# Kernel optimization log

Hardware: AMD Instinct MI355X
Metric: run time of the kernel (lower is better)

Reference implementation:

```python
import jax, jax.numpy as jnp
import numpy as np

TOP_K = 8


def setup_inputs() -> dict:
    key = jax.random.key(0)
    ks = jax.random.split(key, 8)
    B, S, H, BD, N, VBD = 4, 2048, 2048, 256, 256, 256
    return {
        "hidden_states": jax.random.normal(ks[0], (B, S, H), jnp.float32),
        "primary_attention_output": jax.random.normal(ks[1], (B, S, H), jnp.float32),
        "q_proj_w": jax.random.normal(ks[2], (BD, H), jnp.float32) / np.sqrt(H),
        "slot_keys": jax.random.normal(ks[3], (N, BD), jnp.float32),
        "slot_values": jax.random.normal(ks[4], (N, H), jnp.float32),
        "reliability": jax.random.uniform(ks[5], (N,), jnp.float32, 1e-3, 1.0),
        "value_down_w": jax.random.normal(ks[6], (VBD, H), jnp.float32) * 0.1 / np.sqrt(H),
        "value_up_w": jax.random.normal(ks[7], (H, VBD), jnp.float32) * 0.1 / np.sqrt(VBD),
    }


def reference(hidden_states, primary_attention_output, q_proj_w, slot_keys,
              slot_values, reliability, value_down_w, value_up_w):
    B, S, H = hidden_states.shape
    BD = q_proj_w.shape[0]
    # query = q_proj(hidden_states): [B,S,BD]
    query = jnp.einsum("bsh,dh->bsd", hidden_states, q_proj_w)
    # gate-chain scoring: query . slot_keys scaled, plus log-reliability mask
    rel_mask = jnp.log(jnp.clip(reliability, 1e-10))            # [N]
    scores = jnp.einsum("bsd,nd->bsn", query, slot_keys) / jnp.sqrt(
        jnp.asarray(BD, query.dtype)) + rel_mask                # [B,S,N]
    top_scores, top_idx = jax.lax.top_k(scores, TOP_K)          # [B,S,K]
    attn = jax.nn.softmax(top_scores, axis=-1)                  # [B,S,K]
    final_gate = jax.nn.sigmoid(top_scores[..., 0])             # [B,S]
    # slot-pool gather + weighted sum of values (irregular access)
    vals = slot_values[top_idx]                                 # [B,S,K,H]
    aux = jnp.einsum("bsk,bskh->bsh", attn, vals)               # [B,S,H]
    # low-rank value projection with GELU
    aux = jnp.einsum("bsh,vh->bsv", aux, value_down_w)
    aux = jax.nn.gelu(aux)
    aux = jnp.einsum("bsv,hv->bsh", aux, value_up_w)
    return primary_attention_output + final_gate[..., None] * aux
```

## Files before the change

kernel.cpp:

```cpp
#include <hip/hip_runtime.h>
#include <stdint.h>


typedef float f32x4 __attribute__((ext_vector_type(4)));
typedef unsigned short u16x8 __attribute__((ext_vector_type(8)));
typedef unsigned short u16x4 __attribute__((ext_vector_type(4)));
typedef __bf16 bf16x8 __attribute__((ext_vector_type(8)));

#define WS_QW    0u
#define WS_SK    1048576u
#define WS_SV    1179648u
#define WS_VDW   2228224u
#define WS_VUP   3276800u
#define WS_REL   4325376u
#define WS_PV    4326400u
#define WS_GATE  4588544u
#define WS_QP    4621312u
#define WS_D     21398528u

static __device__ __forceinline__ unsigned short f2bf(float f) {
  union { float f; unsigned int u; } v; v.f = f;
  unsigned int r = v.u + 0x7FFFu + ((v.u >> 16) & 1u);
  return (unsigned short)(r >> 16);
}
static __device__ __forceinline__ bf16x8 as_bf16(u16x8 v) {
  return __builtin_bit_cast(bf16x8, v);
}
static __device__ __forceinline__ float gelu_tanh(float x) {
  float u = 0.7978845608028654f * (x + 0.044715f * x * x * x);
  return 0.5f * x * (1.0f + tanhf(u));
}

__global__ void k_prep(const float* __restrict__ qw, const float* __restrict__ sk,
                       const float* __restrict__ sv, const float* __restrict__ vdw,
                       const float* __restrict__ vup, const float* __restrict__ rel,
                       unsigned char* __restrict__ ws) {
  unsigned short* o_qw  = (unsigned short*)(ws + WS_QW);
  unsigned short* o_sk  = (unsigned short*)(ws + WS_SK);
  unsigned short* o_sv  = (unsigned short*)(ws + WS_SV);
  unsigned short* o_vdw = (unsigned short*)(ws + WS_VDW);
  unsigned short* o_vup = (unsigned short*)(ws + WS_VUP);
  float* o_rel = (float*)(ws + WS_REL);
  int tid = blockIdx.x * blockDim.x + threadIdx.x;
  int stride = gridDim.x * blockDim.x;
  for (int g = tid; g < 540736; g += stride) {
    const float* src; unsigned short* dst; int i;
    if      (g < 131072) { src = qw;  dst = o_qw;  i = g; }
    else if (g < 147456) { src = sk;  dst = o_sk;  i = g - 131072; }
    else if (g < 278528) { src = sv;  dst = o_sv;  i = g - 147456; }
    else if (g < 409600) { src = vdw; dst = o_vdw; i = g - 278528; }
    else if (g < 540672) { src = vup; dst = o_vup; i = g - 409600; }
    else {
      int i4 = (g - 540672) * 4;
      #pragma unroll
      for (int j = 0; j < 4; j++) o_rel[i4 + j] = logf(fmaxf(rel[i4 + j], 1e-10f));
      continue;
    }
    f32x4 v = *(const f32x4*)(src + (size_t)i * 4);
    u16x4 o;
    #pragma unroll
    for (int j = 0; j < 4; j++) o[j] = f2bf(v[j]);
    *(u16x4*)(dst + (size_t)i * 4) = o;
  }
}

__global__ __launch_bounds__(256, 2) void k_pv(unsigned char* __restrict__ ws) {
  const unsigned short* sv  = (const unsigned short*)(ws + WS_SV);
  const unsigned short* vdw = (const unsigned short*)(ws + WS_VDW);
  float* PV = (float*)(ws + WS_PV);
  __shared__ __align__(16) unsigned short As[32 * 64];
  __shared__ __align__(16) unsigned short Bs[32 * 64];
  int t = threadIdx.x, lane = t & 63, w = t >> 6;
  int nt = blockIdx.x >> 3, vt = blockIdx.x & 7;
  int mf = w >> 1, nf = w & 1;
  f32x4 acc = {0.f, 0.f, 0.f, 0.f};
  int r = t >> 3, c = t & 7;
  int sw8 = (c ^ (r & 7)) * 8;
  for (int k0 = 0; k0 < 2048; k0 += 64) {
    __syncthreads();
    *(u16x8*)&As[r * 64 + sw8] = *(const u16x8*)&sv[(size_t)(nt * 32 + r) * 2048 + k0 + c * 8];
    *(u16x8*)&Bs[r * 64 + sw8] = *(const u16x8*)&vdw[(size_t)(vt * 32 + r) * 2048 + k0 + c * 8];
    __syncthreads();
    #pragma unroll
    for (int kk = 0; kk < 2; kk++) {
      int ck = kk * 4 + (lane >> 4);
      int ar = mf * 16 + (lane & 15);
      int br = nf * 16 + (lane & 15);
      bf16x8 a = as_bf16(*(const u16x8*)&As[ar * 64 + ((ck ^ (ar & 7)) * 8)]);
      bf16x8 b = as_bf16(*(const u16x8*)&Bs[br * 64 + ((ck ^ (br & 7)) * 8)]);
      acc = __builtin_amdgcn_mfma_f32_16x16x32_bf16(a, b, acc, 0, 0, 0);
    }
  }
  int row = nt * 32 + mf * 16 + (lane >> 4) * 4;
  int col = vt * 32 + nf * 16 + (lane & 15);
  #pragma unroll
  for (int j = 0; j < 4; j++) PV[(row + j) * 256 + col] = acc[j];
}

__global__ __launch_bounds__(256, 4) void k_query(const float* __restrict__ hs,
                                                  unsigned char* __restrict__ ws) {
  const unsigned short* qw = (const unsigned short*)(ws + WS_QW);
  float* qp = (float*)(ws + WS_QP);
  __shared__ __align__(16) unsigned short As[32 * 64];
  __shared__ __align__(16) unsigned short Bs[256 * 64];
  int t = threadIdx.x, lane = t & 63, w = t >> 6;
  int rt = blockIdx.x >> 1, ks = blockIdx.x & 1;
  int row0 = rt * 32, kbase = ks * 1024;
  f32x4 acc[2][4] = {};
  int sr = t >> 3, sc = t & 7;
  const float* aptr = hs + (size_t)(row0 + sr) * 2048 + kbase + sc * 8;
  const unsigned short* bptr = qw + (size_t)sr * 2048 + kbase + sc * 8;
  f32x4 pa0, pa1;
  u16x8 pb0, pb1, pb2, pb3, pb4, pb5, pb6, pb7;
  pa0 = *(const f32x4*)(aptr);
  pa1 = *(const f32x4*)(aptr + 4);
  pb0 = *(const u16x8*)(bptr + (size_t)0 * 32 * 2048);
  pb1 = *(const u16x8*)(bptr + (size_t)1 * 32 * 2048);
  pb2 = *(const u16x8*)(bptr + (size_t)2 * 32 * 2048);
  pb3 = *(const u16x8*)(bptr + (size_t)3 * 32 * 2048);
  pb4 = *(const u16x8*)(bptr + (size_t)4 * 32 * 2048);
  pb5 = *(const u16x8*)(bptr + (size_t)5 * 32 * 2048);
  pb6 = *(const u16x8*)(bptr + (size_t)6 * 32 * 2048);
  pb7 = *(const u16x8*)(bptr + (size_t)7 * 32 * 2048);
  for (int kt = 0; kt < 16; kt++) {
    __syncthreads();
    {
      u16x8 o;
      #pragma unroll
      for (int j = 0; j < 4; j++) { o[j] = f2bf(pa0[j]); o[4 + j] = f2bf(pa1[j]); }
      *(u16x8*)&As[sr * 64 + ((sc ^ (sr & 7)) * 8)] = o;
      u16x8 pb[8] = {pb0, pb1, pb2, pb3, pb4, pb5, pb6, pb7};
      #pragma unroll
      for (int i = 0; i < 8; i++) {
        int n = i * 32 + sr;
        *(u16x8*)&Bs[n * 64 + ((sc ^ (n & 7)) * 8)] = pb[i];
      }
    }
    __syncthreads();
    if (kt < 15) {
      int off = (kt + 1) * 64;
      pa0 = *(const f32x4*)(aptr + off);
      pa1 = *(const f32x4*)(aptr + off + 4);
      pb0 = *(const u16x8*)(bptr + (size_t)0 * 32 * 2048 + off);
      pb1 = *(const u16x8*)(bptr + (size_t)1 * 32 * 2048 + off);
      pb2 = *(const u16x8*)(bptr + (size_t)2 * 32 * 2048 + off);
      pb3 = *(const u16x8*)(bptr + (size_t)3 * 32 * 2048 + off);
      pb4 = *(const u16x8*)(bptr + (size_t)4 * 32 * 2048 + off);
      pb5 = *(const u16x8*)(bptr + (size_t)5 * 32 * 2048 + off);
      pb6 = *(const u16x8*)(bptr + (size_t)6 * 32 * 2048 + off);
      pb7 = *(const u16x8*)(bptr + (size_t)7 * 32 * 2048 + off);
    }
    #pragma unroll
    for (int kk = 0; kk < 2; kk++) {
      int ck = kk * 4 + (lane >> 4);
      bf16x8 a[2], b[4];
      #pragma unroll
      for (int mf = 0; mf < 2; mf++) {
        int arow = mf * 16 + (lane & 15);
        a[mf] = as_bf16(*(const u16x8*)&As[arow * 64 + ((ck ^ (arow & 7)) * 8)]);
      }
      #pragma unroll
      for (int nf = 0; nf < 4; nf++) {
        int brow = w * 64 + nf * 16 + (lane & 15);
        b[nf] = as_bf16(*(const u16x8*)&Bs[brow * 64 + ((ck ^ (brow & 7)) * 8)]);
      }
      #pragma unroll
      for (int mf = 0; mf < 2; mf++)
        #pragma unroll
        for (int nf = 0; nf < 4; nf++)
          acc[mf][nf] = __builtin_amdgcn_mfma_f32_16x16x32_bf16(a[mf], b[nf], acc[mf][nf], 0, 0, 0);
    }
  }
  float* outp = qp + (size_t)ks * 8192 * 256;
  #pragma unroll
  for (int mf = 0; mf < 2; mf++) {
    int row = row0 + mf * 16 + (lane >> 4) * 4;
    #pragma unroll
    for (int nf = 0; nf < 4; nf++) {
      int col = w * 64 + nf * 16 + (lane & 15);
      #pragma unroll
      for (int j = 0; j < 4; j++) outp[(size_t)(row + j) * 256 + col] = acc[mf][nf][j];
    }
  }
}

#define QSTR 264
#define SSTR 260
__global__ __launch_bounds__(256, 4) void k_score(unsigned char* __restrict__ ws) {
  const float* qp = (const float*)(ws + WS_QP);
  const unsigned short* sk = (const unsigned short*)(ws + WS_SK);
  const float* relm = (const float*)(ws + WS_REL);
  const float* PV = (const float*)(ws + WS_PV);
  float* gates = (float*)(ws + WS_GATE);
  unsigned short* D = (unsigned short*)(ws + WS_D);
  __shared__ __align__(16) unsigned short Qs[16 * QSTR];
  __shared__ __align__(16) float Ss[16 * SSTR];
  int t = threadIdx.x, lane = t & 63, w = t >> 6;
  int row0 = blockIdx.x * 16;
  #pragma unroll
  for (int i = 0; i < 4; i++) {
    int id = i * 256 + t, r = id >> 6, c4 = id & 63;
    const float* p0 = qp + (size_t)(row0 + r) * 256 + c4 * 4;
    f32x4 a = *(const f32x4*)p0;
    f32x4 b = *(const f32x4*)(p0 + 8192 * 256);
    u16x4 o;
    #pragma unroll
    for (int j = 0; j < 4; j++) o[j] = f2bf(a[j] + b[j]);
    *(u16x4*)&Qs[r * QSTR + c4 * 4] = o;
  }
  __syncthreads();
  {
    f32x4 acc[4] = {};
    for (int ksb = 0; ksb < 8; ksb++) {
      int ck = lane >> 4;
      bf16x8 a = as_bf16(*(const u16x8*)&Qs[(lane & 15) * QSTR + ksb * 32 + ck * 8]);
      #pragma unroll
      for (int nf = 0; nf < 4; nf++) {
        int n = w * 64 + nf * 16 + (lane & 15);
        bf16x8 b = as_bf16(*(const u16x8*)&sk[(size_t)n * 256 + ksb * 32 + ck * 8]);
        acc[nf] = __builtin_amdgcn_mfma_f32_16x16x32_bf16(a, b, acc[nf], 0, 0, 0);
      }
    }
    #pragma unroll
    for (int nf = 0; nf < 4; nf++) {
      int n = w * 64 + nf * 16 + (lane & 15);
      float rm = relm[n];
      int rr = (lane >> 4) * 4;
      #pragma unroll
      for (int j = 0; j < 4; j++) Ss[(rr + j) * SSTR + n] = acc[nf][j] * 0.0625f + rm;
    }
  }
  __syncthreads();
  for (int rr = 0; rr < 4; rr++) {
    int row = w * 4 + rr;
    f32x4 sv4 = *(const f32x4*)&Ss[row * SSTR + lane * 4];
    unsigned int key[4];
    #pragma unroll
    for (int j = 0; j < 4; j++) {
      unsigned int u = __builtin_bit_cast(unsigned int, sv4[j]);
      unsigned int os = (u & 0x80000000u) ? ~u : (u | 0x80000000u);
      key[j] = (os & 0xFFFFFF00u) | (unsigned int)(255 - (lane * 4 + j));
    }
    unsigned int win[8];
    #pragma unroll
    for (int e = 0; e < 8; e++) {
      unsigned int m01 = key[0] > key[1] ? key[0] : key[1];
      unsigned int m23 = key[2] > key[3] ? key[2] : key[3];
      unsigned int m = m01 > m23 ? m01 : m23;
      #pragma unroll
      for (int d = 1; d < 64; d <<= 1) {
        unsigned int o = (unsigned int)__shfl_xor((int)m, d, 64);
        m = o > m ? o : m;
      }
      win[e] = m;
      #pragma unroll
      for (int j = 0; j < 4; j++) if (key[j] == m) key[j] = 0u;
    }
    float s8[8]; int i8[8];
    #pragma unroll
    for (int e = 0; e < 8; e++) {
      i8[e] = 255 - (int)(win[e] & 0xFFu);
      unsigned int os = win[e] & 0xFFFFFF00u;
      unsigned int u = (os & 0x80000000u) ? (os ^ 0x80000000u) : ~os;
      s8[e] = __builtin_bit_cast(float, u);
    }
    float m0 = s8[0], sum = 0.f, we[8];
    #pragma unroll
    for (int e = 0; e < 8; e++) { we[e] = expf(s8[e] - m0); sum += we[e]; }
    float inv = 1.f / sum;
    f32x4 accv = {0.f, 0.f, 0.f, 0.f};
    #pragma unroll
    for (int e = 0; e < 8; e++) {
      float wk = we[e] * inv;
      f32x4 p = *(const f32x4*)(PV + (size_t)i8[e] * 256 + lane * 4);
      #pragma unroll
      for (int j = 0; j < 4; j++) accv[j] += wk * p[j];
    }
    u16x4 o;
    #pragma unroll
    for (int j = 0; j < 4; j++) o[j] = f2bf(gelu_tanh(accv[j]));
    *(u16x4*)&D[(size_t)(row0 + row) * 256 + lane * 4] = o;
    if (lane == 0) gates[row0 + row] = 1.f / (1.f + expf(-m0));
  }
}

union KOutLds {
  unsigned short AB[12288];
  float stage[32 * 132];
};
__global__ __launch_bounds__(256, 4) void k_out(const float* __restrict__ primary,
                                                float* __restrict__ out,
                                                unsigned char* __restrict__ ws) {
  const unsigned short* D = (const unsigned short*)(ws + WS_D);
  const unsigned short* vup = (const unsigned short*)(ws + WS_VUP);
  const float* gates = (const float*)(ws + WS_GATE);
  __shared__ __align__(16) KOutLds u;
  __shared__ float gate_s[64];
  unsigned short* As = u.AB;
  unsigned short* Bs = u.AB + 4096;
  int t = threadIdx.x, lane = t & 63, w = t >> 6;
  int bid = blockIdx.x;
  int L = (bid & 7) * 256 + (bid >> 3);
  int rt = L >> 4, ct = L & 15;
  int wm = w >> 1, wn = w & 1;
  const float* pbase = primary + (size_t)(rt * 64 + (t >> 5)) * 2048 + ct * 128 + (t & 31) * 4;
  f32x4 pref[2][4];
  #pragma unroll
  for (int i = 0; i < 4; i++)
    pref[0][i] = *(const f32x4*)(pbase + (size_t)(i * 8) * 2048);
  if (t < 64) gate_s[t] = gates[rt * 64 + t];
  f32x4 acc[2][4] = {};
  for (int k0 = 0; k0 < 256; k0 += 64) {
    __syncthreads();
    #pragma unroll
    for (int i = 0; i < 2; i++) {
      int id = i * 256 + t, r = id >> 3, c = id & 7;
      *(u16x8*)&As[r * 64 + ((c ^ (r & 7)) * 8)] =
          *(const u16x8*)&D[(size_t)(rt * 64 + r) * 256 + k0 + c * 8];
    }
    #pragma unroll
    for (int i = 0; i < 4; i++) {
      int id = i * 256 + t, r = id >> 3, c = id & 7;
      *(u16x8*)&Bs[r * 64 + ((c ^ (r & 7)) * 8)] =
          *(const u16x8*)&vup[(size_t)(ct * 128 + r) * 256 + k0 + c * 8];
    }
    __syncthreads();
    #pragma unroll
    for (int kk = 0; kk < 2; kk++) {
      int ck = kk * 4 + (lane >> 4);
      bf16x8 a[2], b[4];
      #pragma unroll
      for (int mf = 0; mf < 2; mf++) {
        int ar = wm * 32 + mf * 16 + (lane & 15);
        a[mf] = as_bf16(*(const u16x8*)&As[ar * 64 + ((ck ^ (ar & 7)) * 8)]);
      }
      #pragma unroll
      for (int nf = 0; nf < 4; nf++) {
        int br = wn * 64 + nf * 16 + (lane & 15);
        b[nf] = as_bf16(*(const u16x8*)&Bs[br * 64 + ((ck ^ (br & 7)) * 8)]);
      }
      #pragma unroll
      for (int mf = 0; mf < 2; mf++)
        #pragma unroll
        for (int nf = 0; nf < 4; nf++)
          acc[mf][nf] = __builtin_amdgcn_mfma_f32_16x16x32_bf16(a[mf], b[nf], acc[mf][nf], 0, 0, 0);
    }
  }
  #pragma unroll
  for (int c = 0; c < 2; c++) {
    __syncthreads();
    if (wm == c) {
      #pragma unroll
      for (int mf = 0; mf < 2; mf++) {
        #pragma unroll
        for (int nf = 0; nf < 4; nf++) {
          int col = wn * 64 + nf * 16 + (lane & 15);
          #pragma unroll
          for (int j = 0; j < 4; j++) {
            int r = mf * 16 + (lane >> 4) * 4 + j;
            u.stage[r * 132 + col] = acc[mf][nf][j];
          }
        }
      }
    }
    if (c == 0) {
      #pragma unroll
      for (int i = 0; i < 4; i++)
        pref[1][i] = *(const f32x4*)(pbase + (size_t)(32 + i * 8) * 2048);
    }
    __syncthreads();
    #pragma unroll
    for (int i = 0; i < 4; i++) {
      int idx = i * 256 + t, r = idx >> 5, c4 = idx & 31;
      int row = rt * 64 + c * 32 + r;
      size_t o = (size_t)row * 2048 + ct * 128 + c4 * 4;
      f32x4 p = pref[c][i];
      f32x4 s = *(const f32x4*)&u.stage[r * 132 + c4 * 4];
      float g = gate_s[c * 32 + r];
      f32x4 ov;
      #pragma unroll
      for (int j = 0; j < 4; j++) ov[j] = p[j] + g * s[j];
      *(f32x4*)(out + o) = ov;
    }
  }
}

extern "C" void kernel_launch(void* const* d_in, const int* in_sizes, int n_in,
                              void* d_out, int out_size, void* d_ws, size_t ws_size,
                              hipStream_t stream) {
  const float* hs      = (const float*)d_in[0];
  const float* primary = (const float*)d_in[1];
  const float* qw      = (const float*)d_in[2];
  const float* sk      = (const float*)d_in[3];
  const float* sv      = (const float*)d_in[4];
  const float* rel     = (const float*)d_in[5];
  const float* vdw     = (const float*)d_in[6];
  const float* vup     = (const float*)d_in[7];
  unsigned char* ws = (unsigned char*)d_ws;
  float* out = (float*)d_out;

  k_prep<<<dim3(256), dim3(256), 0, stream>>>(qw, sk, sv, vdw, vup, rel, ws);
  k_pv<<<dim3(64), dim3(256), 0, stream>>>(ws);
  k_query<<<dim3(512), dim3(256), 0, stream>>>(hs, ws);
  k_score<<<dim3(512), dim3(256), 0, stream>>>(ws);
  k_out<<<dim3(2048), dim3(256), 0, stream>>>(primary, out, ws);
}
```

Baseline: 95.10 us.

## Double-buffer k_out operand tiles with direct global-to-LDS loads

Replaces the register-staged copy of the D and value_up tiles in k_out with global_load_lds transfers straight into LDS. It also double-buffers the tiles so the next K-slice loads while MFMAs run on the current one. The swizzle moves to the global source address so the LDS destination stays lane-contiguous. LDS use doubles and launch bounds drop from 4 to 3 blocks per CU, so occupancy for the memory-bound epilogue falls in exchange for overlapping the GEMM loads.

```diff
diff --git a/kernel.cpp b/kernel.cpp
--- a/kernel.cpp
+++ b/kernel.cpp
@@ -29,6 +29,11 @@
 static __device__ __forceinline__ float gelu_tanh(float x) {
   float u = 0.7978845608028654f * (x + 0.044715f * x * x * x);
   return 0.5f * x * (1.0f + tanhf(u));
+}
+static __device__ __forceinline__ void gl_lds16(const void* g, void* l) {
+  __builtin_amdgcn_global_load_lds(
+      (const __attribute__((address_space(1))) unsigned int*)g,
+      (__attribute__((address_space(3))) unsigned int*)l, 16, 0, 0);
 }
 
 __global__ void k_prep(const float* __restrict__ qw, const float* __restrict__ sk,
@@ -285,10 +290,10 @@
 }
 
 union KOutLds {
-  unsigned short AB[12288];
+  unsigned short bufs[2][12288];
   float stage[32 * 132];
 };
-__global__ __launch_bounds__(256, 4) void k_out(const float* __restrict__ primary,
+__global__ __launch_bounds__(256, 3) void k_out(const float* __restrict__ primary,
                                                 float* __restrict__ out,
                                                 unsigned char* __restrict__ ws) {
   const unsigned short* D = (const unsigned short*)(ws + WS_D);
@@ -296,13 +301,27 @@
   const float* gates = (const float*)(ws + WS_GATE);
   __shared__ __align__(16) KOutLds u;
   __shared__ float gate_s[64];
-  unsigned short* As = u.AB;
-  unsigned short* Bs = u.AB + 4096;
   int t = threadIdx.x, lane = t & 63, w = t >> 6;
   int bid = blockIdx.x;
   int L = (bid & 7) * 256 + (bid >> 3);
   int rt = L >> 4, ct = L & 15;
   int wm = w >> 1, wn = w & 1;
+  int qa0 = (w * 2 + 0) * 64 + lane, qa1 = (w * 2 + 1) * 64 + lane;
+  int ra0 = qa0 >> 3, ra1 = qa1 >> 3;
+  const unsigned short* aSrc0 = D + (size_t)(rt * 64 + ra0) * 256 + ((qa0 & 7) ^ (ra0 & 7)) * 8;
+  const unsigned short* aSrc1 = D + (size_t)(rt * 64 + ra1) * 256 + ((qa1 & 7) ^ (ra1 & 7)) * 8;
+  const unsigned short* bSrc[4];
+  int bBase[4], aBase0 = (w * 2 + 0) * 512, aBase1 = (w * 2 + 1) * 512;
+  #pragma unroll
+  for (int i = 0; i < 4; i++) {
+    int q = (w * 4 + i) * 64 + lane, r = q >> 3;
+    bSrc[i] = vup + (size_t)(ct * 128 + r) * 256 + ((q & 7) ^ (r & 7)) * 8;
+    bBase[i] = 4096 + (w * 4 + i) * 512;
+  }
+  gl_lds16(aSrc0, &u.bufs[0][aBase0]);
+  gl_lds16(aSrc1, &u.bufs[0][aBase1]);
+  #pragma unroll
+  for (int i = 0; i < 4; i++) gl_lds16(bSrc[i], &u.bufs[0][bBase[i]]);
   const float* pbase = primary + (size_t)(rt * 64 + (t >> 5)) * 2048 + ct * 128 + (t & 31) * 4;
   f32x4 pref[2][4];
   #pragma unroll
@@ -310,21 +329,19 @@
     pref[0][i] = *(const f32x4*)(pbase + (size_t)(i * 8) * 2048);
   if (t < 64) gate_s[t] = gates[rt * 64 + t];
   f32x4 acc[2][4] = {};
-  for (int k0 = 0; k0 < 256; k0 += 64) {
-    __syncthreads();
-    #pragma unroll
-    for (int i = 0; i < 2; i++) {
-      int id = i * 256 + t, r = id >> 3, c = id & 7;
-      *(u16x8*)&As[r * 64 + ((c ^ (r & 7)) * 8)] =
-          *(const u16x8*)&D[(size_t)(rt * 64 + r) * 256 + k0 + c * 8];
-    }
-    #pragma unroll
-    for (int i = 0; i < 4; i++) {
-      int id = i * 256 + t, r = id >> 3, c = id & 7;
-      *(u16x8*)&Bs[r * 64 + ((c ^ (r & 7)) * 8)] =
-          *(const u16x8*)&vup[(size_t)(ct * 128 + r) * 256 + k0 + c * 8];
-    }
-    __syncthreads();
+  __syncthreads();
+  int cur = 0;
+  #pragma unroll
+  for (int kt = 0; kt < 4; kt++) {
+    if (kt < 3) {
+      int off = (kt + 1) * 64;
+      gl_lds16(aSrc0 + off, &u.bufs[cur ^ 1][aBase0]);
+      gl_lds16(aSrc1 + off, &u.bufs[cur ^ 1][aBase1]);
+      #pragma unroll
+      for (int i = 0; i < 4; i++) gl_lds16(bSrc[i] + off, &u.bufs[cur ^ 1][bBase[i]]);
+    }
+    const unsigned short* As = u.bufs[cur];
+    const unsigned short* Bs = u.bufs[cur] + 4096;
     #pragma unroll
     for (int kk = 0; kk < 2; kk++) {
       int ck = kk * 4 + (lane >> 4);
@@ -345,6 +362,7 @@
         for (int nf = 0; nf < 4; nf++)
           acc[mf][nf] = __builtin_amdgcn_mfma_f32_16x16x32_bf16(a[mf], b[nf], acc[mf][nf], 0, 0, 0);
     }
+    if (kt < 3) { __syncthreads(); cur ^= 1; }
   }
   #pragma unroll
   for (int c = 0; c < 2; c++) {
```

New measurement: 97.97 us. 1.03x slower.
